# Performance work log

Hardware: AMD Instinct MI355X
Metric: run time of the kernel (lower is better)

## Reference

```python
import jax, jax.numpy as jnp
from jax import lax
import numpy as np

FEAT_STRIDE = 16
PRE_NMS_TOP_N = 2000
POST_NMS_TOP_N = 300
NMS_THRESH = 0.7


def _whctrs(a):
    w = a[2] - a[0] + 1.0
    h = a[3] - a[1] + 1.0
    return w, h, a[0] + 0.5 * (w - 1.0), a[1] + 0.5 * (h - 1.0)


def _mkanchors(ws, hs, x_ctr, y_ctr):
    ws = np.asarray(ws, dtype=np.float64)
    hs = np.asarray(hs, dtype=np.float64)
    return np.stack([x_ctr - 0.5 * (ws - 1.0), y_ctr - 0.5 * (hs - 1.0),
                     x_ctr + 0.5 * (ws - 1.0), y_ctr + 0.5 * (hs - 1.0)], axis=1)


def generate_anchors(base_size=16, ratios=np.array([0.5, 1.0, 2.0]), scales=np.array([8.0, 16.0, 32.0])):
    base = np.array([1.0, 1.0, float(base_size), float(base_size)]) - 1.0
    w, h, xc, yc = _whctrs(base)
    size = w * h
    ws = np.round(np.sqrt(size / ratios))
    hs = np.round(ws * ratios)
    ratio_anchors = _mkanchors(ws, hs, xc, yc)
    out = []
    for i in range(ratio_anchors.shape[0]):
        w_i, h_i, xc_i, yc_i = _whctrs(ratio_anchors[i])
        out.append(_mkanchors(w_i * scales, h_i * scales, xc_i, yc_i))
    return np.vstack(out).astype(np.float32)


ANCHORS = generate_anchors()  # [A=9, 4]
NUM_ANCHORS = ANCHORS.shape[0]


def _nms_keep(boxes, thresh):
    # boxes [N,4], already sorted by descending score; torchvision IoU convention.
    x1, y1, x2, y2 = boxes[:, 0], boxes[:, 1], boxes[:, 2], boxes[:, 3]
    areas = (x2 - x1) * (y2 - y1)
    xx1 = jnp.maximum(x1[:, None], x1[None, :])
    yy1 = jnp.maximum(y1[:, None], y1[None, :])
    xx2 = jnp.minimum(x2[:, None], x2[None, :])
    yy2 = jnp.minimum(y2[:, None], y2[None, :])
    inter = jnp.clip(xx2 - xx1, 0.0) * jnp.clip(yy2 - yy1, 0.0)
    iou = inter / (areas[:, None] + areas[None, :] - inter + 1e-9)
    n = boxes.shape[0]
    # sup[i, j] True => box i (higher score) suppresses later box j
    sup = (iou > thresh) & jnp.triu(jnp.ones((n, n), bool), 1)

    def body(i, keep):
        return keep & ~(keep[i] & sup[i])

    return lax.fori_loop(0, n, body, jnp.ones((n,), bool))


def setup_inputs() -> dict:
    key = jax.random.key(0)
    k1, k2 = jax.random.split(key)
    B, A, H, W = 8, NUM_ANCHORS, 128, 128
    scores = jax.random.normal(k1, (B, 2 * A, H, W), jnp.float32)
    bbox_deltas = jax.random.normal(k2, (B, 4 * A, H, W), jnp.float32) * 0.2
    im_h = float(H * FEAT_STRIDE)
    im_w = float(W * FEAT_STRIDE)
    im_info = jnp.tile(jnp.array([[im_h, im_w, 1.0]], jnp.float32), (B, 1))
    return {"scores": scores, "bbox_deltas": bbox_deltas, "im_info": im_info}


def reference(scores, bbox_deltas, im_info):
    B, _, H, W = scores.shape
    A = NUM_ANCHORS
    # --- anchor generation over the feature grid ---
    sx = jnp.arange(W, dtype=jnp.float32) * FEAT_STRIDE
    sy = jnp.arange(H, dtype=jnp.float32) * FEAT_STRIDE
    gx, gy = jnp.meshgrid(sx, sy)  # 'xy' indexing matches np.meshgrid default
    shifts = jnp.stack([gx.ravel(), gy.ravel(), gx.ravel(), gy.ravel()], axis=1)  # [K,4]
    anchors = (jnp.asarray(ANCHORS)[None, :, :] + shifts[:, None, :]).reshape(-1, 4)  # [K*A,4]

    obj_scores = scores[:, A:].transpose(0, 2, 3, 1).reshape(B, -1)   # [B, K*A]
    deltas = bbox_deltas.transpose(0, 2, 3, 1).reshape(B, -1, 4)      # [B, K*A, 4]

    # --- bbox_transform_inv ---
    widths = anchors[:, 2] - anchors[:, 0] + 1.0
    heights = anchors[:, 3] - anchors[:, 1] + 1.0
    ctr_x = anchors[:, 0] + 0.5 * widths
    ctr_y = anchors[:, 1] + 0.5 * heights
    dx, dy, dw, dh = deltas[..., 0], deltas[..., 1], deltas[..., 2], deltas[..., 3]
    pred_ctr_x = dx * widths + ctr_x
    pred_ctr_y = dy * heights + ctr_y
    pred_w = jnp.exp(dw) * widths
    pred_h = jnp.exp(dh) * heights
    proposals = jnp.stack([pred_ctr_x - 0.5 * pred_w, pred_ctr_y - 0.5 * pred_h,
                           pred_ctr_x + 0.5 * pred_w, pred_ctr_y + 0.5 * pred_h], axis=-1)

    # --- clip_boxes: im_info[b] = (h, w, scale) ---
    max_x = (im_info[:, 1] - 1.0)[:, None]
    max_y = (im_info[:, 0] - 1.0)[:, None]
    proposals = jnp.stack([
        jnp.clip(proposals[..., 0], 0.0, max_x),
        jnp.clip(proposals[..., 1], 0.0, max_y),
        jnp.clip(proposals[..., 2], 0.0, max_x),
        jnp.clip(proposals[..., 3], 0.0, max_y)], axis=-1)

    # --- pre-NMS top-k by score ---
    _, order = lax.top_k(obj_scores, PRE_NMS_TOP_N)                  # [B, pre]
    top_props = jnp.take_along_axis(proposals, order[..., None], axis=1)  # [B, pre, 4]

    # --- per-image greedy NMS (fixed-size, jit-compatible) ---
    keep = jax.vmap(lambda b: _nms_keep(b, NMS_THRESH))(top_props)   # [B, pre] bool
    sel = jnp.argsort(jnp.where(keep, 0, 1), axis=1, stable=True)[:, :POST_NMS_TOP_N]
    valid = jnp.take_along_axis(keep, sel, axis=1)                   # [B, post]
    out_boxes = jnp.take_along_axis(top_props, sel[..., None], axis=1) * valid[..., None].astype(top_props.dtype)

    batch_idx = jnp.broadcast_to(
        jnp.arange(B, dtype=out_boxes.dtype)[:, None, None], (B, POST_NMS_TOP_N, 1))
    return jnp.concatenate([batch_idx, out_boxes], axis=-1)  # [B, post_nms_topN, 5]
```

## Files before the change

kernel.cpp:

```cpp
#include <hip/hip_runtime.h>

#define NB 8
#define NA 9
#define NCELL (128 * 128)
#define NTOT (NCELL * NA)
#define PRE_K 2000
#define POST_K 300
#define CAP2 8192
#define PARTS 18
#define NMS_TH 0.7f

__constant__ float c_aw[NA] = {184.f, 368.f, 736.f, 128.f, 256.f, 512.f, 88.f, 176.f, 352.f};
__constant__ float c_ah[NA] = {96.f, 192.f, 384.f, 128.f, 256.f, 512.f, 176.f, 352.f, 704.f};

__device__ __forceinline__ unsigned int sortable(float s) {
    unsigned int u = __float_as_uint(s);
    return (u & 0x80000000u) ? ~u : (u | 0x80000000u);
}

__device__ __forceinline__ unsigned long long shflx64(unsigned long long v, int m) {
    return __shfl_xor(v, m, 64);
}

__device__ __forceinline__ bool iou_gt(float4 c, float4 jb, float barea) {
    float aarea = __fmul_rn(__fsub_rn(c.z, c.x), __fsub_rn(c.w, c.y));
    float xx1 = fmaxf(c.x, jb.x), yy1 = fmaxf(c.y, jb.y);
    float xx2 = fminf(c.z, jb.z), yy2 = fminf(c.w, jb.w);
    float iw = fmaxf(__fsub_rn(xx2, xx1), 0.0f);
    float ih = fmaxf(__fsub_rn(yy2, yy1), 0.0f);
    float inter = __fmul_rn(iw, ih);
    float denom = __fadd_rn(__fsub_rn(__fadd_rn(aarea, barea), inter), 1e-9f);
    return __fdiv_rn(inter, denom) > NMS_TH;
}

__global__ __launch_bounds__(1024) void hist0_kernel(const float* __restrict__ scores,
                                                     unsigned int* __restrict__ h0out) {
    __shared__ unsigned int h[2048];
    int b = blockIdx.y, tid = threadIdx.x;
    h[tid] = 0; h[tid + 1024] = 0;
    __syncthreads();
    const float4* sp4 = (const float4*)(scores + (size_t)b * 18 * NCELL + (size_t)NA * NCELL);
    int base4 = blockIdx.x * 2048;
#pragma unroll
    for (int e = 0; e < 2; ++e) {
        float4 v = sp4[base4 + e * 1024 + tid];
        atomicAdd(&h[sortable(v.x) >> 21], 1u);
        atomicAdd(&h[sortable(v.y) >> 21], 1u);
        atomicAdd(&h[sortable(v.z) >> 21], 1u);
        atomicAdd(&h[sortable(v.w) >> 21], 1u);
    }
    __syncthreads();
    unsigned int* o = h0out + ((size_t)(b * PARTS + blockIdx.x)) * 2048;
    o[tid] = h[tid];
    o[tid + 1024] = h[tid + 1024];
}

__global__ __launch_bounds__(1024) void select0_kernel(const unsigned int* __restrict__ h0out,
                                                       uint2* __restrict__ state0,
                                                       unsigned int* __restrict__ gh1,
                                                       int* __restrict__ cnt) {
    __shared__ unsigned int wpart[16], wexcl[16];
    __shared__ unsigned int thr[1024];
    int b = blockIdx.x, tid = threadIdx.x;
    int lane = tid & 63, wid = tid >> 6;
    if (tid < 128) gh1[b * 128 + tid] = 0;
    if (tid == 0) cnt[b] = 0;
    unsigned int c0 = 0, c1 = 0;
    for (int p = 0; p < PARTS; ++p) {
        const unsigned int* hp = h0out + ((size_t)(b * PARTS + p)) * 2048;
        uint2 v = *(const uint2*)&hp[2 * tid];
        c0 += v.x; c1 += v.y;
    }
    unsigned int sum = c0 + c1;
#pragma unroll
    for (int off = 1; off < 64; off <<= 1) {
        unsigned int v = __shfl_down(sum, off, 64);
        if (lane + off < 64) sum += v;
    }
    if (lane == 0) wpart[wid] = sum;
    __syncthreads();
    if (tid < 16) {
        unsigned int e = 0;
        for (int w = tid + 1; w < 16; ++w) e += wpart[w];
        wexcl[tid] = e;
    }
    __syncthreads();
    unsigned int self = sum + wexcl[wid];
    thr[tid] = self;
    __syncthreads();
    unsigned int above = (tid < 1023) ? thr[tid + 1] : 0u;
    if (self >= (unsigned)PRE_K && above < (unsigned)PRE_K) {
        if (above + c1 >= (unsigned)PRE_K)
            state0[b] = make_uint2((unsigned)(2 * tid + 1), (unsigned)(PRE_K)-above);
        else
            state0[b] = make_uint2((unsigned)(2 * tid), (unsigned)(PRE_K)-above - c1);
    }
}

__global__ __launch_bounds__(1024) void gatherc_kernel(const float* __restrict__ scores,
                                                       const uint2* __restrict__ state0,
                                                       unsigned int* __restrict__ gh1,
                                                       int* __restrict__ cnt,
                                                       unsigned long long* __restrict__ buf) {
    __shared__ unsigned long long lbuf[2048];
    __shared__ unsigned int h128[128];
    __shared__ int lmisc[2];
    int b = blockIdx.y, tid = threadIdx.x;
    if (tid < 128) h128[tid] = 0;
    if (tid == 0) lmisc[0] = 0;
    __syncthreads();
    unsigned int piv = state0[b].x;
    unsigned int P = piv << 21;
    const float4* sp4 = (const float4*)(scores + (size_t)b * 18 * NCELL + (size_t)NA * NCELL);
    int base4 = blockIdx.x * 2048;
#pragma unroll
    for (int e = 0; e < 2; ++e) {
        int t4 = base4 + e * 1024 + tid;
        float4 v = sp4[t4];
        float el[4] = {v.x, v.y, v.z, v.w};
#pragma unroll
        for (int j = 0; j < 4; ++j) {
            unsigned int u = sortable(el[j]);
            if (u >= P) {
                if ((u >> 21) == piv) atomicAdd(&h128[(u >> 14) & 127u], 1u);
                int idx4 = t4 * 4 + j;
                int a = idx4 >> 14;
                int cell = idx4 & 16383;
                unsigned int i = (unsigned int)cell * 9u + (unsigned int)a;
                int pos = atomicAdd(&lmisc[0], 1);
                if (pos < 2048)
                    lbuf[pos] = ((unsigned long long)u << 32) |
                                (unsigned long long)(0xFFFFFFFFu - i);
            }
        }
    }
    __syncthreads();
    if (tid < 128 && h128[tid]) atomicAdd(&gh1[b * 128 + tid], h128[tid]);
    if (tid == 0) lmisc[1] = atomicAdd(&cnt[b], min(lmisc[0], 2048));
    __syncthreads();
    int m = min(lmisc[0], 2048), gb = lmisc[1];
    for (int t = tid; t < m; t += 1024) {
        int g = gb + t;
        if (g < CAP2) buf[(size_t)b * CAP2 + g] = lbuf[t];
    }
}

#define SHFL_STEP(J)                                                          \
    {                                                                         \
        int d_ = (J) >> 1;                                                    \
        bool keepMax = (((tid & d_) == 0) == (((2u * (unsigned)tid) & k) == 0)); \
        unsigned long long pa = shflx64(va, d_);                              \
        unsigned long long pb = shflx64(vb, d_);                              \
        va = keepMax ? (va > pa ? va : pa) : (va < pa ? va : pa);             \
        vb = keepMax ? (vb > pb ? vb : pb) : (vb < pb ? vb : pb);             \
    }
#define LOCAL_STEP()                                                          \
    {                                                                         \
        bool desc = (((2u * (unsigned)tid) & k) == 0);                        \
        unsigned long long lo = va < vb ? va : vb;                            \
        unsigned long long hi = va < vb ? vb : va;                            \
        va = desc ? hi : lo; vb = desc ? lo : hi;                             \
    }

__global__ __launch_bounds__(1024) void sortdec_kernel(const unsigned long long* __restrict__ buf,
                                                       const int* __restrict__ cnt,
                                                       const uint2* __restrict__ state0,
                                                       const unsigned int* __restrict__ gh1,
                                                       const float* __restrict__ deltas,
                                                       const float* __restrict__ im_info,
                                                       float4* __restrict__ props) {
    __shared__ unsigned long long s[4096];
    __shared__ unsigned int spiv;
    __shared__ int fcnt;
    int b = blockIdx.x, tid = threadIdx.x;
    if (tid == 0) fcnt = 0;
    if (tid < 64) {
        int lane = tid;
        unsigned int c0 = gh1[b * 128 + 2 * lane];
        unsigned int c1 = gh1[b * 128 + 2 * lane + 1];
        unsigned int sum = c0 + c1;
#pragma unroll
        for (int off = 1; off < 64; off <<= 1) {
            unsigned int v = __shfl_down(sum, off, 64);
            if (lane + off < 64) sum += v;
        }
        unsigned int above = __shfl_down(sum, 1, 64);
        if (lane == 63) above = 0;
        unsigned int need0 = state0[b].y;
        if (sum >= need0 && above < need0) {
            unsigned int d = (above + c1 >= need0) ? (unsigned)(2 * lane + 1) : (unsigned)(2 * lane);
            spiv = ((state0[b].x << 7) | d) << 14;
        }
    }
    __syncthreads();
    unsigned int P = spiv;
    int n = min(cnt[b], CAP2);
    const unsigned long long* src = buf + (size_t)b * CAP2;
    for (int t = tid; t < n; t += 1024) {
        unsigned long long e = src[t];
        if ((unsigned int)(e >> 32) >= P) {
            int pos = atomicAdd(&fcnt, 1);
            if (pos < 4096) s[pos] = e;
        }
    }
    __syncthreads();
    int n2 = min(fcnt, 4096);
    int SZ = (n2 <= 2048) ? 2048 : 4096;
    for (int t = tid; t < SZ; t += 1024)
        if (t >= n2) s[t] = 0ULL;
    __syncthreads();
    if (SZ == 2048) {
        unsigned long long va = s[2 * tid], vb = s[2 * tid + 1];
#pragma unroll
        for (unsigned k = 2; k <= 128; k <<= 1) {
#pragma unroll
            for (unsigned j = k >> 1; j >= 2; j >>= 1) SHFL_STEP(j)
            LOCAL_STEP()
        }
        for (unsigned k = 256; k <= 2048; k <<= 1) {
            s[2 * tid] = va; s[2 * tid + 1] = vb;
            __syncthreads();
            for (unsigned j = k >> 1; j >= 128; j >>= 1) {
                for (int t = tid; t < 2048; t += 1024) {
                    int ixj = t ^ (int)j;
                    if (ixj > t) {
                        unsigned long long x = s[t], y = s[ixj];
                        if ((((unsigned)t & k) == 0) ? (x < y) : (x > y)) { s[t] = y; s[ixj] = x; }
                    }
                }
                __syncthreads();
            }
            va = s[2 * tid]; vb = s[2 * tid + 1];
#pragma unroll
            for (unsigned j = 64; j >= 2; j >>= 1) SHFL_STEP(j)
            LOCAL_STEP()
        }
        s[2 * tid] = va; s[2 * tid + 1] = vb;
        __syncthreads();
    } else {
        for (int k = 2; k <= 4096; k <<= 1) {
            for (int j = k >> 1; j > 0; j >>= 1) {
                for (int t = tid; t < 4096; t += 1024) {
                    int ixj = t ^ j;
                    if (ixj > t) {
                        unsigned long long x = s[t], y = s[ixj];
                        if (((t & k) == 0) ? (x < y) : (x > y)) { s[t] = y; s[ixj] = x; }
                    }
                }
                __syncthreads();
            }
        }
    }
    float maxx = __fsub_rn(im_info[b * 3 + 1], 1.0f);
    float maxy = __fsub_rn(im_info[b * 3 + 0], 1.0f);
    const float* dbase = deltas + (size_t)b * 36 * NCELL;
    for (int r = tid; r < PRE_K; r += 1024) {
        unsigned int i = 0xFFFFFFFFu - (unsigned int)(s[r] & 0xFFFFFFFFu);
        unsigned int cell = i / 9u;
        unsigned int a = i - cell * 9u;
        int wx = (int)(cell & 127u), hy = (int)(cell >> 7);
        const float* dp = dbase + (size_t)(4u * a) * NCELL + (size_t)hy * 128 + wx;
        float dx = dp[0];
        float dy = dp[NCELL];
        float dw = dp[2 * NCELL];
        float dh = dp[3 * NCELL];
        float W_ = c_aw[a], H_ = c_ah[a];
        float cx = (float)(16 * wx + 8), cy = (float)(16 * hy + 8);
        float px = __fadd_rn(__fmul_rn(dx, W_), cx);
        float py = __fadd_rn(__fmul_rn(dy, H_), cy);
        float pw = __fmul_rn((float)exp((double)dw), W_);
        float ph = __fmul_rn((float)exp((double)dh), H_);
        float hw = __fmul_rn(0.5f, pw), hh = __fmul_rn(0.5f, ph);
        float x1 = __fsub_rn(px, hw), y1 = __fsub_rn(py, hh);
        float x2 = __fadd_rn(px, hw), y2 = __fadd_rn(py, hh);
        x1 = fminf(fmaxf(x1, 0.0f), maxx);
        y1 = fminf(fmaxf(y1, 0.0f), maxy);
        x2 = fminf(fmaxf(x2, 0.0f), maxx);
        y2 = fminf(fmaxf(y2, 0.0f), maxy);
        props[(size_t)b * PRE_K + r] = make_float4(x1, y1, x2, y2);
    }
}

__global__ __launch_bounds__(1024) void nms_kernel(const float4* __restrict__ props,
                                                   float* __restrict__ out) {
    __shared__ float4 sbox[PRE_K];
    __shared__ float4 kbox[POST_K];
    __shared__ unsigned long long colpart[16][64];
    __shared__ unsigned long long deadmask[16];
    __shared__ int ctl[2];
    int b = blockIdx.x, tid = threadIdx.x;
    int jl = tid & 63, w = tid >> 6;
    for (int t = tid; t < PRE_K; t += 1024) sbox[t] = props[(size_t)b * PRE_K + t];
    if (tid == 0) { ctl[0] = 0; ctl[1] = 0; }
    __syncthreads();
    for (int k = 0; k < 32; ++k) {
        int j = k * 64 + jl;
        bool jvalid = j < PRE_K;
        float4 jb = jvalid ? sbox[j] : make_float4(0.f, 0.f, -1.f, -1.f);
        float barea = __fmul_rn(__fsub_rn(jb.z, jb.x), __fsub_rn(jb.w, jb.y));
        int T = ctl[0];
        bool dead = false;
        if (jvalid) {
            for (int i = w; i < T; i += 16) {
                if (iou_gt(kbox[i], jb, barea)) { dead = true; break; }
            }
        }
        deadmask[w] = __ballot(dead);
        unsigned long long part = 0ULL;
        if (jvalid) {
#pragma unroll
            for (int q = 0; q < 4; ++q) {
                int ii = 4 * w + q;
                if (ii < jl) {
                    if (iou_gt(sbox[k * 64 + ii], jb, barea)) part |= (1ULL << ii);
                }
            }
        }
        colpart[w][jl] = part;
        __syncthreads();
        if (w == 0) {
            unsigned long long d = deadmask[0];
            unsigned long long diag = colpart[0][jl];
#pragma unroll
            for (int x = 1; x < 16; ++x) { d |= deadmask[x]; diag |= colpart[x][jl]; }
            bool mydead = ((d >> jl) & 1ULL) != 0ULL;
            unsigned long long alive = __ballot(!mydead && jvalid);
            unsigned long long keptw = 0ULL;
            int total = ctl[0];
            int done = 0;
            while (alive) {
                int i = __builtin_ctzll(alive);
                keptw |= (1ULL << i);
                if (jl == 0 && total < POST_K) kbox[total] = sbox[k * 64 + i];
                total++;
                if (total >= POST_K) { done = 1; break; }
                unsigned long long sup = __ballot(((diag >> i) & 1ULL) != 0ULL);
                alive &= ~sup;
                alive &= ~keptw;
            }
            if (jl == 0) { ctl[0] = total; ctl[1] = done; }
        }
        __syncthreads();
        if (ctl[1]) break;
    }
    __syncthreads();
    int K = min(ctl[0], POST_K);
    for (int r = tid; r < POST_K; r += 1024) {
        float4 v = make_float4(0.f, 0.f, 0.f, 0.f);
        if (r < K) v = kbox[r];
        float* o = out + ((size_t)b * POST_K + r) * 5;
        o[0] = (float)b;
        o[1] = v.x;
        o[2] = v.y;
        o[3] = v.z;
        o[4] = v.w;
    }
}

extern "C" void kernel_launch(void* const* d_in, const int* in_sizes, int n_in,
                              void* d_out, int out_size, void* d_ws, size_t ws_size,
                              hipStream_t stream) {
    const float* scores = (const float*)d_in[0];
    const float* deltas = (const float*)d_in[1];
    const float* im_info = (const float*)d_in[2];
    float* out = (float*)d_out;
    char* ws = (char*)d_ws;

    unsigned int* h0out = (unsigned int*)(ws + 0);
    unsigned int* gh1 = (unsigned int*)(ws + 1179648);
    uint2* state0 = (uint2*)(ws + 1183744);
    int* cnt = (int*)(ws + 1183808);
    unsigned long long* buf = (unsigned long long*)(ws + 1183872);
    float4* props = (float4*)(ws + 1708160);

    hipLaunchKernelGGL(hist0_kernel, dim3(PARTS, NB), dim3(1024), 0, stream, scores, h0out);
    hipLaunchKernelGGL(select0_kernel, dim3(NB), dim3(1024), 0, stream, h0out, state0, gh1, cnt);
    hipLaunchKernelGGL(gatherc_kernel, dim3(PARTS, NB), dim3(1024), 0, stream,
                       scores, state0, gh1, cnt, buf);
    hipLaunchKernelGGL(sortdec_kernel, dim3(NB), dim3(1024), 0, stream,
                       buf, cnt, state0, gh1, deltas, im_info, props);
    hipLaunchKernelGGL(nms_kernel, dim3(NB), dim3(1024), 0, stream, props, out);
}
```

Measured before the change: 100.7 us.

## Split NMS into parallel IoU bitmask kernel and single-wave scan kernel

Replaces the single-block-per-image greedy NMS with a two-stage scheme. The first stage computes upper-triangular IoU suppression bitmasks for all box pairs across a large grid. The second stage has one wave per image scan the bitmasks to select kept boxes and gather them from global memory. This targets the poor parallelism of using only eight blocks, at the cost of computing the full pairwise triangle instead of only comparing against kept boxes, plus an extra global buffer and launch.

```diff
diff --git a/kernel.cpp b/kernel.cpp
--- a/kernel.cpp
+++ b/kernel.cpp
@@ -20,17 +20,6 @@
 
 __device__ __forceinline__ unsigned long long shflx64(unsigned long long v, int m) {
     return __shfl_xor(v, m, 64);
-}
-
-__device__ __forceinline__ bool iou_gt(float4 c, float4 jb, float barea) {
-    float aarea = __fmul_rn(__fsub_rn(c.z, c.x), __fsub_rn(c.w, c.y));
-    float xx1 = fmaxf(c.x, jb.x), yy1 = fmaxf(c.y, jb.y);
-    float xx2 = fminf(c.z, jb.z), yy2 = fminf(c.w, jb.w);
-    float iw = fmaxf(__fsub_rn(xx2, xx1), 0.0f);
-    float ih = fmaxf(__fsub_rn(yy2, yy1), 0.0f);
-    float inter = __fmul_rn(iw, ih);
-    float denom = __fadd_rn(__fsub_rn(__fadd_rn(aarea, barea), inter), 1e-9f);
-    return __fdiv_rn(inter, denom) > NMS_TH;
 }
 
 __global__ __launch_bounds__(1024) void hist0_kernel(const float* __restrict__ scores,
@@ -281,73 +270,83 @@
     }
 }
 
-__global__ __launch_bounds__(1024) void nms_kernel(const float4* __restrict__ props,
-                                                   float* __restrict__ out) {
-    __shared__ float4 sbox[PRE_K];
-    __shared__ float4 kbox[POST_K];
-    __shared__ unsigned long long colpart[16][64];
-    __shared__ unsigned long long deadmask[16];
-    __shared__ int ctl[2];
-    int b = blockIdx.x, tid = threadIdx.x;
-    int jl = tid & 63, w = tid >> 6;
-    for (int t = tid; t < PRE_K; t += 1024) sbox[t] = props[(size_t)b * PRE_K + t];
-    if (tid == 0) { ctl[0] = 0; ctl[1] = 0; }
-    __syncthreads();
-    for (int k = 0; k < 32; ++k) {
-        int j = k * 64 + jl;
-        bool jvalid = j < PRE_K;
-        float4 jb = jvalid ? sbox[j] : make_float4(0.f, 0.f, -1.f, -1.f);
-        float barea = __fmul_rn(__fsub_rn(jb.z, jb.x), __fsub_rn(jb.w, jb.y));
-        int T = ctl[0];
-        bool dead = false;
-        if (jvalid) {
-            for (int i = w; i < T; i += 16) {
-                if (iou_gt(kbox[i], jb, barea)) { dead = true; break; }
-            }
-        }
-        deadmask[w] = __ballot(dead);
-        unsigned long long part = 0ULL;
-        if (jvalid) {
-#pragma unroll
-            for (int q = 0; q < 4; ++q) {
-                int ii = 4 * w + q;
-                if (ii < jl) {
-                    if (iou_gt(sbox[k * 64 + ii], jb, barea)) part |= (1ULL << ii);
-                }
-            }
-        }
-        colpart[w][jl] = part;
+__global__ void mask_kernel(const float4* __restrict__ boxes,
+                            unsigned long long* __restrict__ colm) {
+    int iT = blockIdx.x, jT = blockIdx.y, b = blockIdx.z;
+    if (iT > jT) return;
+    __shared__ float4 ib[64];
+    int t = threadIdx.x;
+    int i0 = iT * 64;
+    ib[t] = (i0 + t < PRE_K) ? boxes[(size_t)b * PRE_K + i0 + t] : make_float4(0.f, 0.f, -1.f, -1.f);
+    __syncthreads();
+    int j = jT * 64 + t;
+    if (j >= PRE_K) return;
+    float4 jb = boxes[(size_t)b * PRE_K + j];
+    float barea = __fmul_rn(__fsub_rn(jb.z, jb.x), __fsub_rn(jb.w, jb.y));
+    unsigned long long m = 0ULL;
+    for (int ii = 0; ii < 64; ++ii) {
+        int i = i0 + ii;
+        if (i < j) {
+            float4 c = ib[ii];
+            float aarea = __fmul_rn(__fsub_rn(c.z, c.x), __fsub_rn(c.w, c.y));
+            float xx1 = fmaxf(c.x, jb.x), yy1 = fmaxf(c.y, jb.y);
+            float xx2 = fminf(c.z, jb.z), yy2 = fminf(c.w, jb.w);
+            float iw = fmaxf(__fsub_rn(xx2, xx1), 0.0f);
+            float ih = fmaxf(__fsub_rn(yy2, yy1), 0.0f);
+            float inter = __fmul_rn(iw, ih);
+            float denom = __fadd_rn(__fsub_rn(__fadd_rn(aarea, barea), inter), 1e-9f);
+            float iou = __fdiv_rn(inter, denom);
+            if (iou > NMS_TH) m |= (1ULL << ii);
+        }
+    }
+    colm[((size_t)b * 32 + iT) * 2048 + j] = m;
+}
+
+__global__ void scan_kernel(const unsigned long long* __restrict__ colm,
+                            const float4* __restrict__ boxes,
+                            float* __restrict__ out) {
+    int b = blockIdx.x;
+    int lane = threadIdx.x;
+    __shared__ unsigned long long kw[32];
+    __shared__ int keeplist[POST_K];
+    const unsigned long long* cb = colm + (size_t)b * 32 * 2048;
+    int total = 0;
+    bool done = false;
+    for (int k = 0; k < 32 && !done; ++k) {
+        int j = k * 64 + lane;
+        unsigned long long d = 0;
+        int w = 0;
+        for (; w + 4 <= k; w += 4) {
+            unsigned long long a0 = cb[(size_t)(w + 0) * 2048 + j] & kw[w + 0];
+            unsigned long long a1 = cb[(size_t)(w + 1) * 2048 + j] & kw[w + 1];
+            unsigned long long a2 = cb[(size_t)(w + 2) * 2048 + j] & kw[w + 2];
+            unsigned long long a3 = cb[(size_t)(w + 3) * 2048 + j] & kw[w + 3];
+            d |= (a0 | a1) | (a2 | a3);
+        }
+        for (; w < k; ++w) d |= cb[(size_t)w * 2048 + j] & kw[w];
+        unsigned long long diag = cb[(size_t)k * 2048 + j];
+        bool alive_me = (d == 0ULL) && (j < PRE_K);
+        unsigned long long alive = __ballot(alive_me);
+        unsigned long long keptw = 0ULL;
+        while (alive) {
+            int i = __builtin_ctzll(alive);
+            keptw |= (1ULL << i);
+            if (lane == 0 && total < POST_K) keeplist[total] = k * 64 + i;
+            total++;
+            if (total >= POST_K) { done = true; break; }
+            unsigned long long sup = __ballot(((diag >> i) & 1ULL) != 0ULL);
+            alive &= ~sup;
+            alive &= ~keptw;
+        }
+        if (lane == 0) kw[k] = keptw;
         __syncthreads();
-        if (w == 0) {
-            unsigned long long d = deadmask[0];
-            unsigned long long diag = colpart[0][jl];
-#pragma unroll
-            for (int x = 1; x < 16; ++x) { d |= deadmask[x]; diag |= colpart[x][jl]; }
-            bool mydead = ((d >> jl) & 1ULL) != 0ULL;
-            unsigned long long alive = __ballot(!mydead && jvalid);
-            unsigned long long keptw = 0ULL;
-            int total = ctl[0];
-            int done = 0;
-            while (alive) {
-                int i = __builtin_ctzll(alive);
-                keptw |= (1ULL << i);
-                if (jl == 0 && total < POST_K) kbox[total] = sbox[k * 64 + i];
-                total++;
-                if (total >= POST_K) { done = 1; break; }
-                unsigned long long sup = __ballot(((diag >> i) & 1ULL) != 0ULL);
-                alive &= ~sup;
-                alive &= ~keptw;
-            }
-            if (jl == 0) { ctl[0] = total; ctl[1] = done; }
-        }
-        __syncthreads();
-        if (ctl[1]) break;
-    }
-    __syncthreads();
-    int K = min(ctl[0], POST_K);
-    for (int r = tid; r < POST_K; r += 1024) {
+    }
+    __syncthreads();
+    int K = min(total, POST_K);
+    const float4* bb = boxes + (size_t)b * PRE_K;
+    for (int r = lane; r < POST_K; r += 64) {
         float4 v = make_float4(0.f, 0.f, 0.f, 0.f);
-        if (r < K) v = kbox[r];
+        if (r < K) v = bb[keeplist[r]];
         float* o = out + ((size_t)b * POST_K + r) * 5;
         o[0] = (float)b;
         o[1] = v.x;
@@ -372,6 +371,7 @@
     int* cnt = (int*)(ws + 1183808);
     unsigned long long* buf = (unsigned long long*)(ws + 1183872);
     float4* props = (float4*)(ws + 1708160);
+    unsigned long long* colm = (unsigned long long*)(ws + 1966080);
 
     hipLaunchKernelGGL(hist0_kernel, dim3(PARTS, NB), dim3(1024), 0, stream, scores, h0out);
     hipLaunchKernelGGL(select0_kernel, dim3(NB), dim3(1024), 0, stream, h0out, state0, gh1, cnt);
@@ -379,5 +379,6 @@
                        scores, state0, gh1, cnt, buf);
     hipLaunchKernelGGL(sortdec_kernel, dim3(NB), dim3(1024), 0, stream,
                        buf, cnt, state0, gh1, deltas, im_info, props);
-    hipLaunchKernelGGL(nms_kernel, dim3(NB), dim3(1024), 0, stream, props, out);
-}
+    hipLaunchKernelGGL(mask_kernel, dim3(32, 32, NB), dim3(64), 0, stream, props, colm);
+    hipLaunchKernelGGL(scan_kernel, dim3(NB), dim3(64), 0, stream, colm, props, out);
+}
```

Result: slower. 103.3 us (+2.6%).
